# Kernel tuning notes

Measured on AMD Instinct MI355X. Metric: run time of the kernel, lower is better.

The kernel has to match this reference:

```python
import jax, jax.numpy as jnp
import numpy as np

HIDDEN = 128
N_NODES = 50000
N_EDGES = 640000


def setup_inputs() -> dict:
    key = jax.random.key(0)
    k1, k2, k3, k4, k5, k6, k7 = jax.random.split(key, 7)
    z = jax.random.normal(k1, (N_NODES, HIDDEN), dtype=jnp.float32)
    edge_index = jax.random.randint(k2, (2, N_EDGES), 0, N_NODES, dtype=jnp.int64)
    # Linear params (torch default uniform(-1/sqrt(fan_in), 1/sqrt(fan_in)))
    b1 = 1.0 / np.sqrt(2 * HIDDEN)
    W1 = jax.random.uniform(k3, (HIDDEN, 2 * HIDDEN), jnp.float32, -b1, b1)
    bias1 = jax.random.uniform(k4, (HIDDEN,), jnp.float32, -b1, b1)
    b2 = 1.0 / np.sqrt(HIDDEN)
    W2 = jax.random.uniform(k5, (1, HIDDEN), jnp.float32, -b2, b2)
    bias2 = jax.random.uniform(k6, (1,), jnp.float32, -b2, b2)
    return {"z": z, "W1": W1, "bias1": bias1, "W2": W2, "bias2": bias2,
            "edge_index": edge_index}


def reference(z, W1, bias1, W2, bias2, edge_index):
    # Gather endpoint embeddings: [E, H] each
    z_src = z[edge_index[0]]
    z_dst = z[edge_index[1]]
    h = jnp.concatenate([z_src, z_dst], axis=-1)  # [E, 2H]
    h = jax.nn.relu(h @ W1.T + bias1)             # [E, H]
    out = h @ W2.T + bias2                        # [E, 1]
    return out.reshape(-1)
```

## Files before the change

### kernel.cpp

```cpp
#include <hip/hip_runtime.h>
#include <hip/hip_bf16.h>


#define N_NODES 50000
#define N_EDGES 640000
#define H 128

using bf16 = __hip_bfloat16;
typedef __attribute__((ext_vector_type(8))) short short8;
typedef __attribute__((ext_vector_type(4))) float f32x4;

#define GLD_LDS16(g, l)                                                     \
  __builtin_amdgcn_global_load_lds(                                         \
      (const __attribute__((address_space(1))) void*)(g),                   \
      (__attribute__((address_space(3))) void*)(l), 16, 0, 0)

static __device__ __forceinline__ short bfbits(float x) {
  __hip_bfloat16 h = __float2bfloat16(x);
  return *reinterpret_cast<short*>(&h);
}

static __device__ __forceinline__ short8 pack8(float4 a, float4 b) {
  short8 r;
  r[0] = bfbits(a.x); r[1] = bfbits(a.y); r[2] = bfbits(a.z); r[3] = bfbits(a.w);
  r[4] = bfbits(b.x); r[5] = bfbits(b.y); r[6] = bfbits(b.z); r[7] = bfbits(b.w);
  return r;
}

__global__ __launch_bounds__(256) void w_to_bf16(const float* __restrict__ W1,
                                                 bf16* __restrict__ Wb) {
  const int u = blockIdx.x * 256 + threadIdx.x;
  const int o = u >> 4, k8 = (u & 15) * 8;
  const float4* src = reinterpret_cast<const float4*>(
      W1 + (size_t)(o & (H - 1)) * (2 * H) + (o >> 7) * H + k8);
  *reinterpret_cast<short8*>(Wb + (size_t)o * H + k8) = pack8(src[0], src[1]);
}

#define HP 136

__global__ __launch_bounds__(256) void precompute_uv(
    const float* __restrict__ z, const bf16* __restrict__ Wb,
    bf16* __restrict__ U, bf16* __restrict__ V) {
  __shared__ float ldsF[32 * H];
  __shared__ bf16 ldsH[32 * HP];
  const int tid = threadIdx.x;
  const int lane = tid & 63;
  const int s = tid >> 6;
  const int l15 = lane & 15, quad = lane >> 4;
  const int nodebase = blockIdx.x * 32;

  {
    int r0 = nodebase + s * 8;
    if (r0 > N_NODES - 8) r0 = N_NODES - 8;
    const float* gsrc = z + (size_t)r0 * H + lane * 4;
    float* ldst = ldsF + s * 8 * H;
#pragma unroll
    for (int j = 0; j < 4; ++j) GLD_LDS16(gsrc + j * 256, ldst + j * 256);
  }

  short8 wf[4][4];
#pragma unroll
  for (int t = 0; t < 4; ++t) {
    const bf16* wp = Wb + (size_t)(s * 64 + t * 16 + l15) * H + quad * 8;
#pragma unroll
    for (int q = 0; q < 4; ++q)
      wf[t][q] = *reinterpret_cast<const short8*>(wp + q * 32);
  }

  __syncthreads();

  {
    const int row = tid >> 3, off = (tid & 7) * 16;
    const float4* fp = reinterpret_cast<const float4*>(ldsF + row * H + off);
    const float4 a = fp[0], b = fp[1], c = fp[2], d = fp[3];
    *reinterpret_cast<short8*>(&ldsH[row * HP + off]) = pack8(a, b);
    *reinterpret_cast<short8*>(&ldsH[row * HP + off + 8]) = pack8(c, d);
  }
  __syncthreads();

  short8 zf[2][4];
#pragma unroll
  for (int m = 0; m < 2; ++m)
#pragma unroll
    for (int q = 0; q < 4; ++q)
      zf[m][q] = *reinterpret_cast<const short8*>(
          &ldsH[(m * 16 + l15) * HP + quad * 8 + q * 32]);

  f32x4 acc[2][4] = {};
#pragma unroll
  for (int m = 0; m < 2; ++m)
#pragma unroll
    for (int t = 0; t < 4; ++t)
#pragma unroll
      for (int q = 0; q < 4; ++q)
        acc[m][t] =
            __builtin_amdgcn_mfma_f32_16x16x32_bf16(wf[t][q], zf[m][q], acc[m][t], 0, 0, 0);

  bf16* epi = reinterpret_cast<bf16*>(ldsF);
#pragma unroll
  for (int m = 0; m < 2; ++m) {
    const int nl = m * 16 + l15;
#pragma unroll
    for (int t = 0; t < 4; ++t) {
      const int o = s * 64 + t * 16 + quad * 4;
      ushort4 st;
      st.x = (unsigned short)bfbits(acc[m][t][0]);
      st.y = (unsigned short)bfbits(acc[m][t][1]);
      st.z = (unsigned short)bfbits(acc[m][t][2]);
      st.w = (unsigned short)bfbits(acc[m][t][3]);
      *reinterpret_cast<ushort4*>(epi + nl * 256 + o) = st;
    }
  }
  __syncthreads();

#pragma unroll
  for (int half = 0; half < 2; ++half) {
    bf16* base = half ? V : U;
#pragma unroll
    for (int it = 0; it < 2; ++it) {
      const int nl = s * 8 + it * 4 + (lane >> 4);
      const int oc = (lane & 15) * 8;
      const short8 v = *reinterpret_cast<const short8*>(epi + nl * 256 + half * H + oc);
      const int n = nodebase + nl;
      if (n < N_NODES)
        *reinterpret_cast<short8*>(base + (size_t)n * H + oc) = v;
    }
  }
}

static __device__ __forceinline__ void acc2(unsigned u, unsigned v,
                                            float b1lo, float b1hi,
                                            float w2lo, float w2hi, float& sum) {
  const float ulo = __uint_as_float(u << 16);
  const float uhi = __uint_as_float(u & 0xffff0000u);
  const float vlo = __uint_as_float(v << 16);
  const float vhi = __uint_as_float(v & 0xffff0000u);
  float h0 = ulo + vlo + b1lo; h0 = fmaxf(h0, 0.f);
  float h1 = uhi + vhi + b1hi; h1 = fmaxf(h1, 0.f);
  sum = fmaf(h0, w2lo, sum);
  sum = fmaf(h1, w2hi, sum);
}

__global__ __launch_bounds__(256, 4) void edge_decode(
    const int* __restrict__ eidx, const bf16* __restrict__ Ub,
    const bf16* __restrict__ Vb, const float* __restrict__ bias1,
    const float* __restrict__ W2, const float* __restrict__ bias2,
    float* __restrict__ out) {
  const int lane = threadIdx.x & 63;
  const int w = blockIdx.x * 4 + (int)(threadIdx.x >> 6);
  const int chunk = w * 64;
  const int e8 = lane & 7;

  float b1r[16], w2r[16];
  const float4* bp = reinterpret_cast<const float4*>(bias1 + e8 * 16);
  const float4* wp = reinterpret_cast<const float4*>(W2 + e8 * 16);
#pragma unroll
  for (int q = 0; q < 4; ++q) {
    const float4 b = bp[q], wv = wp[q];
    b1r[q * 4 + 0] = b.x; b1r[q * 4 + 1] = b.y; b1r[q * 4 + 2] = b.z; b1r[q * 4 + 3] = b.w;
    w2r[q * 4 + 0] = wv.x; w2r[q * 4 + 1] = wv.y; w2r[q * 4 + 2] = wv.z; w2r[q * 4 + 3] = wv.w;
  }
  const float b2 = bias2[0];

  const int src = eidx[chunk + lane];
  const int dst = eidx[N_EDGES + chunk + lane];
  const uint4* U4 = reinterpret_cast<const uint4*>(Ub);
  const uint4* V4 = reinterpret_cast<const uint4*>(Vb);

  float res = 0.f;
#pragma unroll
  for (int half = 0; half < 2; ++half) {
    uint4 ua[4], ub[4], va[4], vb[4];
#pragma unroll
    for (int j = 0; j < 4; ++j) {
      const int i = half * 4 + j;
      const int sl = (lane & 56) + i;
      const int s_i = __shfl(src, sl);
      const int d_i = __shfl(dst, sl);
      const uint4* up = U4 + (size_t)s_i * 16 + e8 * 2;
      const uint4* vp = V4 + (size_t)d_i * 16 + e8 * 2;
      ua[j] = up[0]; ub[j] = up[1];
      va[j] = vp[0]; vb[j] = vp[1];
    }
#pragma unroll
    for (int j = 0; j < 4; ++j) {
      const int i = half * 4 + j;
      float sum = 0.f;
      acc2(ua[j].x, va[j].x, b1r[0],  b1r[1],  w2r[0],  w2r[1],  sum);
      acc2(ua[j].y, va[j].y, b1r[2],  b1r[3],  w2r[2],  w2r[3],  sum);
      acc2(ua[j].z, va[j].z, b1r[4],  b1r[5],  w2r[4],  w2r[5],  sum);
      acc2(ua[j].w, va[j].w, b1r[6],  b1r[7],  w2r[6],  w2r[7],  sum);
      acc2(ub[j].x, vb[j].x, b1r[8],  b1r[9],  w2r[8],  w2r[9],  sum);
      acc2(ub[j].y, vb[j].y, b1r[10], b1r[11], w2r[10], w2r[11], sum);
      acc2(ub[j].z, vb[j].z, b1r[12], b1r[13], w2r[12], w2r[13], sum);
      acc2(ub[j].w, vb[j].w, b1r[14], b1r[15], w2r[14], w2r[15], sum);
      sum += __shfl_xor(sum, 1);
      sum += __shfl_xor(sum, 2);
      sum += __shfl_xor(sum, 4);
      if (e8 == i) res = sum + b2;
    }
  }
  out[chunk + lane] = res;
}

extern "C" void kernel_launch(void* const* d_in, const int* in_sizes, int n_in,
                              void* d_out, int out_size, void* d_ws, size_t ws_size,
                              hipStream_t stream) {
  const float* z     = (const float*)d_in[0];
  const float* W1    = (const float*)d_in[1];
  const float* bias1 = (const float*)d_in[2];
  const float* W2    = (const float*)d_in[3];
  const float* bias2 = (const float*)d_in[4];
  const int*   eidx  = (const int*)d_in[5];
  float* out = (float*)d_out;

  bf16* U  = (bf16*)d_ws;
  bf16* V  = U + (size_t)N_NODES * H;
  bf16* Wb = V + (size_t)N_NODES * H;

  hipLaunchKernelGGL(w_to_bf16, dim3(16), dim3(256), 0, stream, W1, Wb);
  hipLaunchKernelGGL(precompute_uv, dim3((N_NODES + 31) / 32), dim3(256), 0, stream,
                     z, Wb, U, V);
  hipLaunchKernelGGL(edge_decode, dim3(N_EDGES / 64 / 4), dim3(256), 0, stream,
                     eidx, U, V, bias1, W2, bias2, out);
}
```

Measured before the change: 136.6 us.

## Bin edges by endpoint ranges and schedule decode per XCD for L2 locality

Adds a histogram, scan and scatter pass that buckets edges by coarse (dst, src) node ranges into 256 bins, packing src, dst and edge id into 64-bit records. The decode kernel then assigns each group of 32 bins to one XCD (blockIdx & 7) so each XCD's L2 sees a smaller working set of U/V rows, aiming to reduce random gather traffic to HBM. This costs three extra kernels, a memset and atomics, extra global traffic for the sorted records, and scattered output writes. It also assumes node ids fit in 16 bits and that blocks map round-robin to XCDs.

```diff
diff --git a/kernel.cpp b/kernel.cpp
--- a/kernel.cpp
+++ b/kernel.cpp
@@ -5,6 +5,11 @@
 #define N_NODES 50000
 #define N_EDGES 640000
 #define H 128
+
+#define NBINS 256
+#define S1_BLOCKS 128
+#define EPT 20
+#define P_XCD 64
 
 using bf16 = __hip_bfloat16;
 typedef __attribute__((ext_vector_type(8))) short short8;
@@ -124,6 +129,84 @@
       const int n = nodebase + nl;
       if (n < N_NODES)
         *reinterpret_cast<short8*>(base + (size_t)n * H + oc) = v;
+    }
+  }
+}
+
+
+static __device__ __forceinline__ int edge_key(int src, int dst) {
+  return (dst / 6250) * 32 + src / 1563;
+}
+
+__global__ __launch_bounds__(256) void edge_hist(const int* __restrict__ eidx,
+                                                 int* __restrict__ hist) {
+  __shared__ int lh[NBINS];
+  const int t = threadIdx.x;
+  lh[t] = 0;
+  __syncthreads();
+  const int base = blockIdx.x * (256 * EPT) + t;
+#pragma unroll
+  for (int j = 0; j < EPT; ++j) {
+    const int e = base + j * 256;
+    if (e < N_EDGES)
+      atomicAdd(&lh[edge_key(eidx[e], eidx[N_EDGES + e])], 1);
+  }
+  __syncthreads();
+  if (lh[t]) atomicAdd(&hist[t * 16], lh[t]);
+}
+
+__global__ __launch_bounds__(256) void edge_scan(const int* __restrict__ hist,
+                                                 int* __restrict__ cursors,
+                                                 int* __restrict__ xstart) {
+  __shared__ int sh[NBINS];
+  const int t = threadIdx.x;
+  const int v = hist[t * 16];
+  int acc = v;
+  sh[t] = acc;
+  for (int off = 1; off < NBINS; off <<= 1) {
+    __syncthreads();
+    const int add = (t >= off) ? sh[t - off] : 0;
+    __syncthreads();
+    acc += add;
+    sh[t] = acc;
+  }
+  const int excl = acc - v;
+  cursors[t * 16] = excl;
+  if ((t & 31) == 0) xstart[t >> 5] = excl;
+  if (t == 0) xstart[8] = N_EDGES;
+}
+
+__global__ __launch_bounds__(256) void edge_scatter(
+    const int* __restrict__ eidx, int* __restrict__ cursors,
+    unsigned long long* __restrict__ sde) {
+  __shared__ int lh[NBINS];
+  __shared__ int lcur[NBINS];
+  const int t = threadIdx.x;
+  lh[t] = 0;
+  __syncthreads();
+  int src[EPT], dst[EPT], key[EPT];
+  const int base = blockIdx.x * (256 * EPT) + t;
+#pragma unroll
+  for (int j = 0; j < EPT; ++j) {
+    const int e = base + j * 256;
+    if (e < N_EDGES) {
+      src[j] = eidx[e];
+      dst[j] = eidx[N_EDGES + e];
+      key[j] = edge_key(src[j], dst[j]);
+      atomicAdd(&lh[key[j]], 1);
+    } else {
+      key[j] = -1;
+    }
+  }
+  __syncthreads();
+  lcur[t] = lh[t] ? atomicAdd(&cursors[t * 16], lh[t]) : 0;
+  __syncthreads();
+#pragma unroll
+  for (int j = 0; j < EPT; ++j) {
+    if (key[j] >= 0) {
+      const int pos = atomicAdd(&lcur[key[j]], 1);
+      sde[pos] = ((unsigned long long)(unsigned)(base + j * 256) << 32) |
+                 ((unsigned)dst[j] << 16) | (unsigned)src[j];
     }
   }
 }
@@ -141,14 +224,12 @@
   sum = fmaf(h1, w2hi, sum);
 }
 
-__global__ __launch_bounds__(256, 4) void edge_decode(
-    const int* __restrict__ eidx, const bf16* __restrict__ Ub,
+__global__ __launch_bounds__(256, 4) void edge_decode_sorted(
+    const unsigned long long* __restrict__ sde, const bf16* __restrict__ Ub,
     const bf16* __restrict__ Vb, const float* __restrict__ bias1,
     const float* __restrict__ W2, const float* __restrict__ bias2,
-    float* __restrict__ out) {
+    const int* __restrict__ xstart, float* __restrict__ out) {
   const int lane = threadIdx.x & 63;
-  const int w = blockIdx.x * 4 + (int)(threadIdx.x >> 6);
-  const int chunk = w * 64;
   const int e8 = lane & 7;
 
   float b1r[16], w2r[16];
@@ -162,45 +243,56 @@
   }
   const float b2 = bias2[0];
 
-  const int src = eidx[chunk + lane];
-  const int dst = eidx[N_EDGES + chunk + lane];
+  const int xcd = blockIdx.x & 7;
+  const int slot = blockIdx.x >> 3;
+  const int xs = xstart[xcd], xe = xstart[xcd + 1];
   const uint4* U4 = reinterpret_cast<const uint4*>(Ub);
   const uint4* V4 = reinterpret_cast<const uint4*>(Vb);
 
-  float res = 0.f;
-#pragma unroll
-  for (int half = 0; half < 2; ++half) {
-    uint4 ua[4], ub[4], va[4], vb[4];
-#pragma unroll
-    for (int j = 0; j < 4; ++j) {
-      const int i = half * 4 + j;
-      const int sl = (lane & 56) + i;
-      const int s_i = __shfl(src, sl);
-      const int d_i = __shfl(dst, sl);
-      const uint4* up = U4 + (size_t)s_i * 16 + e8 * 2;
-      const uint4* vp = V4 + (size_t)d_i * 16 + e8 * 2;
-      ua[j] = up[0]; ub[j] = up[1];
-      va[j] = vp[0]; vb[j] = vp[1];
-    }
-#pragma unroll
-    for (int j = 0; j < 4; ++j) {
-      const int i = half * 4 + j;
-      float sum = 0.f;
-      acc2(ua[j].x, va[j].x, b1r[0],  b1r[1],  w2r[0],  w2r[1],  sum);
-      acc2(ua[j].y, va[j].y, b1r[2],  b1r[3],  w2r[2],  w2r[3],  sum);
-      acc2(ua[j].z, va[j].z, b1r[4],  b1r[5],  w2r[4],  w2r[5],  sum);
-      acc2(ua[j].w, va[j].w, b1r[6],  b1r[7],  w2r[6],  w2r[7],  sum);
-      acc2(ub[j].x, vb[j].x, b1r[8],  b1r[9],  w2r[8],  w2r[9],  sum);
-      acc2(ub[j].y, vb[j].y, b1r[10], b1r[11], w2r[10], w2r[11], sum);
-      acc2(ub[j].z, vb[j].z, b1r[12], b1r[13], w2r[12], w2r[13], sum);
-      acc2(ub[j].w, vb[j].w, b1r[14], b1r[15], w2r[14], w2r[15], sum);
-      sum += __shfl_xor(sum, 1);
-      sum += __shfl_xor(sum, 2);
-      sum += __shfl_xor(sum, 4);
-      if (e8 == i) res = sum + b2;
-    }
-  }
-  out[chunk + lane] = res;
+  for (int cb = xs + (slot * 4 + (int)(threadIdx.x >> 6)) * 64; cb < xe;
+       cb += P_XCD * 256) {
+    const int idx = cb + lane;
+    const bool valid = idx < xe;
+    const unsigned long long v = valid ? sde[idx] : 0ull;
+    const int src = (int)(v & 0xFFFFu);
+    const int dst = (int)((v >> 16) & 0xFFFFu);
+    const int eid = (int)(v >> 32);
+
+    float res = 0.f;
+#pragma unroll
+    for (int half = 0; half < 2; ++half) {
+      uint4 ua[4], ub[4], va[4], vb[4];
+#pragma unroll
+      for (int j = 0; j < 4; ++j) {
+        const int i = half * 4 + j;
+        const int sl = (lane & 56) + i;
+        const int s_i = __shfl(src, sl);
+        const int d_i = __shfl(dst, sl);
+        const uint4* up = U4 + (size_t)s_i * 16 + e8 * 2;
+        const uint4* vp = V4 + (size_t)d_i * 16 + e8 * 2;
+        ua[j] = up[0]; ub[j] = up[1];
+        va[j] = vp[0]; vb[j] = vp[1];
+      }
+#pragma unroll
+      for (int j = 0; j < 4; ++j) {
+        const int i = half * 4 + j;
+        float sum = 0.f;
+        acc2(ua[j].x, va[j].x, b1r[0],  b1r[1],  w2r[0],  w2r[1],  sum);
+        acc2(ua[j].y, va[j].y, b1r[2],  b1r[3],  w2r[2],  w2r[3],  sum);
+        acc2(ua[j].z, va[j].z, b1r[4],  b1r[5],  w2r[4],  w2r[5],  sum);
+        acc2(ua[j].w, va[j].w, b1r[6],  b1r[7],  w2r[6],  w2r[7],  sum);
+        acc2(ub[j].x, vb[j].x, b1r[8],  b1r[9],  w2r[8],  w2r[9],  sum);
+        acc2(ub[j].y, vb[j].y, b1r[10], b1r[11], w2r[10], w2r[11], sum);
+        acc2(ub[j].z, vb[j].z, b1r[12], b1r[13], w2r[12], w2r[13], sum);
+        acc2(ub[j].w, vb[j].w, b1r[14], b1r[15], w2r[14], w2r[15], sum);
+        sum += __shfl_xor(sum, 1);
+        sum += __shfl_xor(sum, 2);
+        sum += __shfl_xor(sum, 4);
+        if (e8 == i) res = sum + b2;
+      }
+    }
+    if (valid) out[eid] = res;
+  }
 }
 
 extern "C" void kernel_launch(void* const* d_in, const int* in_sizes, int n_in,
@@ -217,10 +309,20 @@
   bf16* U  = (bf16*)d_ws;
   bf16* V  = U + (size_t)N_NODES * H;
   bf16* Wb = V + (size_t)N_NODES * H;
+  unsigned long long* sde = (unsigned long long*)(Wb + 256 * H);
+  int* hist    = (int*)(sde + N_EDGES);
+  int* cursors = hist + NBINS * 16;
+  int* xstart  = cursors + NBINS * 16;
+
+  hipMemsetAsync(hist, 0, NBINS * 16 * sizeof(int), stream);
 
   hipLaunchKernelGGL(w_to_bf16, dim3(16), dim3(256), 0, stream, W1, Wb);
   hipLaunchKernelGGL(precompute_uv, dim3((N_NODES + 31) / 32), dim3(256), 0, stream,
                      z, Wb, U, V);
-  hipLaunchKernelGGL(edge_decode, dim3(N_EDGES / 64 / 4), dim3(256), 0, stream,
-                     eidx, U, V, bias1, W2, bias2, out);
-}
+  hipLaunchKernelGGL(edge_hist, dim3(S1_BLOCKS), dim3(256), 0, stream, eidx, hist);
+  hipLaunchKernelGGL(edge_scan, dim3(1), dim3(256), 0, stream, hist, cursors, xstart);
+  hipLaunchKernelGGL(edge_scatter, dim3(S1_BLOCKS), dim3(256), 0, stream,
+                     eidx, cursors, sde);
+  hipLaunchKernelGGL(edge_decode_sorted, dim3(8 * P_XCD), dim3(256), 0, stream,
+                     sde, U, V, bias1, W2, bias2, xstart, out);
+}
```

Result: slower. 154.8 us (+13.3%).

## Bucket edges by source node to reuse U rows in edge decoding

Applied to the files above, without the earlier changes.

Adds a bucketing kernel that groups edges by source node into fixed-capacity slots with an overflow list. The decode kernel then walks nodes in a grid-stride loop, loads each source U row once and reuses it across that node's edges, gathering only V rows per edge. The aim is to halve the random row gathers. In exchange it pays for a memset, atomics, an extra kernel and scattered output writes, and the per-node loop has divergent trip counts. Packing the destination index into 16 bits truncates node ids of 65536 and above; with 50000 nodes this holds.

```diff
diff --git a/kernel.cpp b/kernel.cpp
--- a/kernel.cpp
+++ b/kernel.cpp
@@ -5,6 +5,9 @@
 #define N_NODES 50000
 #define N_EDGES 640000
 #define H 128
+
+#define CAP 64
+#define OVF_MAX 65536
 
 using bf16 = __hip_bfloat16;
 typedef __attribute__((ext_vector_type(8))) short short8;
@@ -125,6 +128,25 @@
       if (n < N_NODES)
         *reinterpret_cast<short8*>(base + (size_t)n * H + oc) = v;
     }
+  }
+}
+
+__global__ __launch_bounds__(256) void build_buckets(
+    const int* __restrict__ eidx, int* __restrict__ cnt, int* __restrict__ ovfn,
+    unsigned long long* __restrict__ slots,
+    unsigned long long* __restrict__ ovfl) {
+  const int e = blockIdx.x * 256 + threadIdx.x;
+  if (e >= N_EDGES) return;
+  const unsigned s = (unsigned)eidx[e];
+  const unsigned d = (unsigned)eidx[N_EDGES + e];
+  const unsigned long long p =
+      ((unsigned long long)(unsigned)e << 32) | (d << 16) | s;
+  const int pos = atomicAdd(&cnt[s], 1);
+  if (pos < CAP) {
+    slots[(size_t)s * CAP + pos] = p;
+  } else {
+    const int op = atomicAdd(ovfn, 1);
+    if (op < OVF_MAX) ovfl[op] = p;
   }
 }
 
@@ -141,15 +163,30 @@
   sum = fmaf(h1, w2hi, sum);
 }
 
-__global__ __launch_bounds__(256, 4) void edge_decode(
-    const int* __restrict__ eidx, const bf16* __restrict__ Ub,
-    const bf16* __restrict__ Vb, const float* __restrict__ bias1,
-    const float* __restrict__ W2, const float* __restrict__ bias2,
-    float* __restrict__ out) {
-  const int lane = threadIdx.x & 63;
-  const int w = blockIdx.x * 4 + (int)(threadIdx.x >> 6);
-  const int chunk = w * 64;
-  const int e8 = lane & 7;
+static __device__ __forceinline__ float edge_sum(const uint4& a0, const uint4& a1,
+                                                 const uint4& c0, const uint4& c1,
+                                                 const float* b1r, const float* w2r) {
+  float sum = 0.f;
+  acc2(a0.x, c0.x, b1r[0],  b1r[1],  w2r[0],  w2r[1],  sum);
+  acc2(a0.y, c0.y, b1r[2],  b1r[3],  w2r[2],  w2r[3],  sum);
+  acc2(a0.z, c0.z, b1r[4],  b1r[5],  w2r[4],  w2r[5],  sum);
+  acc2(a0.w, c0.w, b1r[6],  b1r[7],  w2r[6],  w2r[7],  sum);
+  acc2(a1.x, c1.x, b1r[8],  b1r[9],  w2r[8],  w2r[9],  sum);
+  acc2(a1.y, c1.y, b1r[10], b1r[11], w2r[10], w2r[11], sum);
+  acc2(a1.z, c1.z, b1r[12], b1r[13], w2r[12], w2r[13], sum);
+  acc2(a1.w, c1.w, b1r[14], b1r[15], w2r[14], w2r[15], sum);
+  return sum;
+}
+
+__global__ __launch_bounds__(256, 4) void edge_decode_csr(
+    const unsigned long long* __restrict__ slots, const int* __restrict__ cnt,
+    const int* __restrict__ ovfn, const unsigned long long* __restrict__ ovfl,
+    const bf16* __restrict__ Ub, const bf16* __restrict__ Vb,
+    const float* __restrict__ bias1, const float* __restrict__ W2,
+    const float* __restrict__ bias2, float* __restrict__ out) {
+  const int e8 = threadIdx.x & 7;
+  const int g = (blockIdx.x * 256 + threadIdx.x) >> 3;
+  const int n_groups = gridDim.x * 32;
 
   float b1r[16], w2r[16];
   const float4* bp = reinterpret_cast<const float4*>(bias1 + e8 * 16);
@@ -162,45 +199,61 @@
   }
   const float b2 = bias2[0];
 
-  const int src = eidx[chunk + lane];
-  const int dst = eidx[N_EDGES + chunk + lane];
   const uint4* U4 = reinterpret_cast<const uint4*>(Ub);
   const uint4* V4 = reinterpret_cast<const uint4*>(Vb);
 
-  float res = 0.f;
-#pragma unroll
-  for (int half = 0; half < 2; ++half) {
-    uint4 ua[4], ub[4], va[4], vb[4];
-#pragma unroll
-    for (int j = 0; j < 4; ++j) {
-      const int i = half * 4 + j;
-      const int sl = (lane & 56) + i;
-      const int s_i = __shfl(src, sl);
-      const int d_i = __shfl(dst, sl);
-      const uint4* up = U4 + (size_t)s_i * 16 + e8 * 2;
-      const uint4* vp = V4 + (size_t)d_i * 16 + e8 * 2;
-      ua[j] = up[0]; ub[j] = up[1];
-      va[j] = vp[0]; vb[j] = vp[1];
+  for (int n = g; n < N_NODES; n += n_groups) {
+    const int deg = min(cnt[n], CAP);
+    if (deg == 0) continue;
+    const uint4* up = U4 + (size_t)n * 16 + e8 * 2;
+    const uint4 u0 = up[0], u1 = up[1];
+    const unsigned long long* sb = slots + (size_t)n * CAP;
+
+    for (int j0 = 0; j0 < deg; j0 += 4) {
+      const int m = deg - j0;
+      unsigned long long ent = 0;
+      if ((e8 & 3) < m) ent = sb[j0 + (e8 & 3)];
+      uint4 va[4], vb[4];
+      int eid[4];
+#pragma unroll
+      for (int j = 0; j < 4; ++j) {
+        const unsigned long long pj = __shfl(ent, (threadIdx.x & 56) | j);
+        if (j < m) {
+          const int dj = (int)((pj >> 16) & 0xffffu);
+          eid[j] = (int)(pj >> 32);
+          const uint4* vp = V4 + (size_t)dj * 16 + e8 * 2;
+          va[j] = vp[0];
+          vb[j] = vp[1];
+        }
+      }
+#pragma unroll
+      for (int j = 0; j < 4; ++j) {
+        if (j < m) {
+          float sum = edge_sum(u0, u1, va[j], vb[j], b1r, w2r);
+          sum += __shfl_xor(sum, 1);
+          sum += __shfl_xor(sum, 2);
+          sum += __shfl_xor(sum, 4);
+          if (e8 == j) out[eid[j]] = sum + b2;
+        }
+      }
     }
-#pragma unroll
-    for (int j = 0; j < 4; ++j) {
-      const int i = half * 4 + j;
-      float sum = 0.f;
-      acc2(ua[j].x, va[j].x, b1r[0],  b1r[1],  w2r[0],  w2r[1],  sum);
-      acc2(ua[j].y, va[j].y, b1r[2],  b1r[3],  w2r[2],  w2r[3],  sum);
-      acc2(ua[j].z, va[j].z, b1r[4],  b1r[5],  w2r[4],  w2r[5],  sum);
-      acc2(ua[j].w, va[j].w, b1r[6],  b1r[7],  w2r[6],  w2r[7],  sum);
-      acc2(ub[j].x, vb[j].x, b1r[8],  b1r[9],  w2r[8],  w2r[9],  sum);
-      acc2(ub[j].y, vb[j].y, b1r[10], b1r[11], w2r[10], w2r[11], sum);
-      acc2(ub[j].z, vb[j].z, b1r[12], b1r[13], w2r[12], w2r[13], sum);
-      acc2(ub[j].w, vb[j].w, b1r[14], b1r[15], w2r[14], w2r[15], sum);
-      sum += __shfl_xor(sum, 1);
-      sum += __shfl_xor(sum, 2);
-      sum += __shfl_xor(sum, 4);
-      if (e8 == i) res = sum + b2;
-    }
-  }
-  out[chunk + lane] = res;
+  }
+
+  const int no = min(*ovfn, OVF_MAX);
+  for (int i = g; i < no; i += n_groups) {
+    const unsigned long long p = ovfl[i];
+    const int s = (int)(p & 0xffffu);
+    const int d = (int)((p >> 16) & 0xffffu);
+    const int eid0 = (int)(p >> 32);
+    const uint4* up2 = U4 + (size_t)s * 16 + e8 * 2;
+    const uint4* vp2 = V4 + (size_t)d * 16 + e8 * 2;
+    const uint4 a0 = up2[0], a1 = up2[1], c0 = vp2[0], c1 = vp2[1];
+    float sum = edge_sum(a0, a1, c0, c1, b1r, w2r);
+    sum += __shfl_xor(sum, 1);
+    sum += __shfl_xor(sum, 2);
+    sum += __shfl_xor(sum, 4);
+    if (e8 == 0) out[eid0] = sum + b2;
+  }
 }
 
 extern "C" void kernel_launch(void* const* d_in, const int* in_sizes, int n_in,
@@ -217,10 +270,20 @@
   bf16* U  = (bf16*)d_ws;
   bf16* V  = U + (size_t)N_NODES * H;
   bf16* Wb = V + (size_t)N_NODES * H;
+  unsigned long long* slots =
+      (unsigned long long*)(Wb + 256 * H);
+  int* cnt  = (int*)(slots + (size_t)N_NODES * CAP);
+  int* ovfn = cnt + 50048;
+  unsigned long long* ovfl =
+      (unsigned long long*)(cnt + 50064);
+
+  hipMemsetAsync(cnt, 0, 50064 * sizeof(int), stream);
 
   hipLaunchKernelGGL(w_to_bf16, dim3(16), dim3(256), 0, stream, W1, Wb);
   hipLaunchKernelGGL(precompute_uv, dim3((N_NODES + 31) / 32), dim3(256), 0, stream,
                      z, Wb, U, V);
-  hipLaunchKernelGGL(edge_decode, dim3(N_EDGES / 64 / 4), dim3(256), 0, stream,
-                     eidx, U, V, bias1, W2, bias2, out);
-}
+  hipLaunchKernelGGL(build_buckets, dim3((N_EDGES + 255) / 256), dim3(256), 0,
+                     stream, eidx, cnt, ovfn, slots, ovfl);
+  hipLaunchKernelGGL(edge_decode_csr, dim3(512), dim3(256), 0, stream,
+                     slots, cnt, ovfn, ovfl, U, V, bias1, W2, bias2, out);
+}
```

Result: slower. 202.7 us (+48.3%).

## Bin edges by src/dst node range and map bins to XCDs for L2 locality

Applied to the files above, without the earlier changes.

Adds a scatter pass that buckets edges into 256 bins keyed by destination and source node ranges, packing src, dst and edge id into 64-bit entries. The W conversion is folded into the same launch. The decode kernel then processes bins with block-to-XCD mapping so each XCD's L2 sees a limited slice of the U/V tables, and an overflow list catches bins that exceed capacity. The aim is to raise cache hit rates on the random U/V gathers, at the cost of an extra pass over edges, atomics, a memset and scattered output writes.

```diff
diff --git a/kernel.cpp b/kernel.cpp
--- a/kernel.cpp
+++ b/kernel.cpp
@@ -5,6 +5,13 @@
 #define N_NODES 50000
 #define N_EDGES 640000
 #define H 128
+
+#define NBINS 256
+#define CAPB 3072
+#define CHUNKS_PER_BIN 12
+#define SCAT_BLOCKS 128
+#define EPT 20
+#define OVF_MAX 65536
 
 using bf16 = __hip_bfloat16;
 typedef __attribute__((ext_vector_type(8))) short short8;
@@ -25,15 +32,6 @@
   r[0] = bfbits(a.x); r[1] = bfbits(a.y); r[2] = bfbits(a.z); r[3] = bfbits(a.w);
   r[4] = bfbits(b.x); r[5] = bfbits(b.y); r[6] = bfbits(b.z); r[7] = bfbits(b.w);
   return r;
-}
-
-__global__ __launch_bounds__(256) void w_to_bf16(const float* __restrict__ W1,
-                                                 bf16* __restrict__ Wb) {
-  const int u = blockIdx.x * 256 + threadIdx.x;
-  const int o = u >> 4, k8 = (u & 15) * 8;
-  const float4* src = reinterpret_cast<const float4*>(
-      W1 + (size_t)(o & (H - 1)) * (2 * H) + (o >> 7) * H + k8);
-  *reinterpret_cast<short8*>(Wb + (size_t)o * H + k8) = pack8(src[0], src[1]);
 }
 
 #define HP 136
@@ -124,6 +122,57 @@
       const int n = nodebase + nl;
       if (n < N_NODES)
         *reinterpret_cast<short8*>(base + (size_t)n * H + oc) = v;
+    }
+  }
+}
+
+__global__ __launch_bounds__(256) void scatter_w(
+    const int* __restrict__ eidx, const float* __restrict__ W1,
+    bf16* __restrict__ Wb, int* __restrict__ cursors, int* __restrict__ ovfn,
+    unsigned long long* __restrict__ sde,
+    unsigned long long* __restrict__ ovfl) {
+  if (blockIdx.x >= SCAT_BLOCKS) {
+    const int u = (blockIdx.x - SCAT_BLOCKS) * 256 + threadIdx.x;
+    const int o = u >> 4, k8 = (u & 15) * 8;
+    const float4* src = reinterpret_cast<const float4*>(
+        W1 + (size_t)(o & (H - 1)) * (2 * H) + (o >> 7) * H + k8);
+    *reinterpret_cast<short8*>(Wb + (size_t)o * H + k8) = pack8(src[0], src[1]);
+    return;
+  }
+  __shared__ int lh[NBINS];
+  __shared__ int lcur[NBINS];
+  const int t = threadIdx.x;
+  lh[t] = 0;
+  __syncthreads();
+  unsigned long long ent[EPT];
+  int key[EPT];
+  const int base = blockIdx.x * (256 * EPT) + t;
+#pragma unroll
+  for (int j = 0; j < EPT; ++j) {
+    const int e = base + j * 256;
+    if (e < N_EDGES) {
+      const unsigned s = (unsigned)eidx[e];
+      const unsigned d = (unsigned)eidx[N_EDGES + e];
+      ent[j] = ((unsigned long long)(unsigned)e << 32) | (d << 16) | s;
+      key[j] = (int)(d / 6250u) * 32 + (int)(s / 1563u);
+      atomicAdd(&lh[key[j]], 1);
+    } else {
+      key[j] = -1;
+    }
+  }
+  __syncthreads();
+  lcur[t] = lh[t] ? atomicAdd(&cursors[t * 16], lh[t]) : 0;
+  __syncthreads();
+#pragma unroll
+  for (int j = 0; j < EPT; ++j) {
+    if (key[j] >= 0) {
+      const int pos = atomicAdd(&lcur[key[j]], 1);
+      if (pos < CAPB) {
+        sde[(size_t)key[j] * CAPB + pos] = ent[j];
+      } else {
+        const int op = atomicAdd(ovfn, 1);
+        if (op < OVF_MAX) ovfl[op] = ent[j];
+      }
     }
   }
 }
@@ -141,31 +190,31 @@
   sum = fmaf(h1, w2hi, sum);
 }
 
-__global__ __launch_bounds__(256, 4) void edge_decode(
-    const int* __restrict__ eidx, const bf16* __restrict__ Ub,
-    const bf16* __restrict__ Vb, const float* __restrict__ bias1,
-    const float* __restrict__ W2, const float* __restrict__ bias2,
-    float* __restrict__ out) {
-  const int lane = threadIdx.x & 63;
-  const int w = blockIdx.x * 4 + (int)(threadIdx.x >> 6);
-  const int chunk = w * 64;
-  const int e8 = lane & 7;
-
-  float b1r[16], w2r[16];
-  const float4* bp = reinterpret_cast<const float4*>(bias1 + e8 * 16);
-  const float4* wp = reinterpret_cast<const float4*>(W2 + e8 * 16);
-#pragma unroll
-  for (int q = 0; q < 4; ++q) {
-    const float4 b = bp[q], wv = wp[q];
-    b1r[q * 4 + 0] = b.x; b1r[q * 4 + 1] = b.y; b1r[q * 4 + 2] = b.z; b1r[q * 4 + 3] = b.w;
-    w2r[q * 4 + 0] = wv.x; w2r[q * 4 + 1] = wv.y; w2r[q * 4 + 2] = wv.z; w2r[q * 4 + 3] = wv.w;
-  }
-  const float b2 = bias2[0];
-
-  const int src = eidx[chunk + lane];
-  const int dst = eidx[N_EDGES + chunk + lane];
-  const uint4* U4 = reinterpret_cast<const uint4*>(Ub);
-  const uint4* V4 = reinterpret_cast<const uint4*>(Vb);
+static __device__ __forceinline__ float edge_sum(const uint4& a0, const uint4& a1,
+                                                 const uint4& c0, const uint4& c1,
+                                                 const float* b1r, const float* w2r) {
+  float sum = 0.f;
+  acc2(a0.x, c0.x, b1r[0],  b1r[1],  w2r[0],  w2r[1],  sum);
+  acc2(a0.y, c0.y, b1r[2],  b1r[3],  w2r[2],  w2r[3],  sum);
+  acc2(a0.z, c0.z, b1r[4],  b1r[5],  w2r[4],  w2r[5],  sum);
+  acc2(a0.w, c0.w, b1r[6],  b1r[7],  w2r[6],  w2r[7],  sum);
+  acc2(a1.x, c1.x, b1r[8],  b1r[9],  w2r[8],  w2r[9],  sum);
+  acc2(a1.y, c1.y, b1r[10], b1r[11], w2r[10], w2r[11], sum);
+  acc2(a1.z, c1.z, b1r[12], b1r[13], w2r[12], w2r[13], sum);
+  acc2(a1.w, c1.w, b1r[14], b1r[15], w2r[14], w2r[15], sum);
+  return sum;
+}
+
+static __device__ __forceinline__ void decode64(
+    const unsigned long long* __restrict__ ents, int mvalid,
+    const uint4* __restrict__ U4, const uint4* __restrict__ V4,
+    const float* b1r, const float* w2r, float b2, float* __restrict__ out,
+    int lane, int e8) {
+  const bool valid = lane < mvalid;
+  const unsigned long long v = valid ? ents[lane] : 0ull;
+  const int src = (int)(v & 0xffffu);
+  const int dst = (int)((v >> 16) & 0xffffu);
+  const int eid = (int)(v >> 32);
 
   float res = 0.f;
 #pragma unroll
@@ -174,7 +223,7 @@
 #pragma unroll
     for (int j = 0; j < 4; ++j) {
       const int i = half * 4 + j;
-      const int sl = (lane & 56) + i;
+      const int sl = (lane & 56) | i;
       const int s_i = __shfl(src, sl);
       const int d_i = __shfl(dst, sl);
       const uint4* up = U4 + (size_t)s_i * 16 + e8 * 2;
@@ -185,22 +234,54 @@
 #pragma unroll
     for (int j = 0; j < 4; ++j) {
       const int i = half * 4 + j;
-      float sum = 0.f;
-      acc2(ua[j].x, va[j].x, b1r[0],  b1r[1],  w2r[0],  w2r[1],  sum);
-      acc2(ua[j].y, va[j].y, b1r[2],  b1r[3],  w2r[2],  w2r[3],  sum);
-      acc2(ua[j].z, va[j].z, b1r[4],  b1r[5],  w2r[4],  w2r[5],  sum);
-      acc2(ua[j].w, va[j].w, b1r[6],  b1r[7],  w2r[6],  w2r[7],  sum);
-      acc2(ub[j].x, vb[j].x, b1r[8],  b1r[9],  w2r[8],  w2r[9],  sum);
-      acc2(ub[j].y, vb[j].y, b1r[10], b1r[11], w2r[10], w2r[11], sum);
-      acc2(ub[j].z, vb[j].z, b1r[12], b1r[13], w2r[12], w2r[13], sum);
-      acc2(ub[j].w, vb[j].w, b1r[14], b1r[15], w2r[14], w2r[15], sum);
+      float sum = edge_sum(ua[j], ub[j], va[j], vb[j], b1r, w2r);
       sum += __shfl_xor(sum, 1);
       sum += __shfl_xor(sum, 2);
       sum += __shfl_xor(sum, 4);
       if (e8 == i) res = sum + b2;
     }
   }
-  out[chunk + lane] = res;
+  if (valid) out[eid] = res;
+}
+
+__global__ __launch_bounds__(256, 4) void edge_decode_sorted(
+    const unsigned long long* __restrict__ sde, const int* __restrict__ cursors,
+    const int* __restrict__ ovfn, const unsigned long long* __restrict__ ovfl,
+    const bf16* __restrict__ Ub, const bf16* __restrict__ Vb,
+    const float* __restrict__ bias1, const float* __restrict__ W2,
+    const float* __restrict__ bias2, float* __restrict__ out) {
+  const int lane = threadIdx.x & 63;
+  const int e8 = lane & 7;
+  const int w = threadIdx.x >> 6;
+
+  float b1r[16], w2r[16];
+  const float4* bp = reinterpret_cast<const float4*>(bias1 + e8 * 16);
+  const float4* wp = reinterpret_cast<const float4*>(W2 + e8 * 16);
+#pragma unroll
+  for (int q = 0; q < 4; ++q) {
+    const float4 b = bp[q], wv = wp[q];
+    b1r[q * 4 + 0] = b.x; b1r[q * 4 + 1] = b.y; b1r[q * 4 + 2] = b.z; b1r[q * 4 + 3] = b.w;
+    w2r[q * 4 + 0] = wv.x; w2r[q * 4 + 1] = wv.y; w2r[q * 4 + 2] = wv.z; w2r[q * 4 + 3] = wv.w;
+  }
+  const float b2 = bias2[0];
+
+  const uint4* U4 = reinterpret_cast<const uint4*>(Ub);
+  const uint4* V4 = reinterpret_cast<const uint4*>(Vb);
+
+  const int xcd = blockIdx.x & 7;
+  const int slot = blockIdx.x >> 3;
+  const int sb = slot / CHUNKS_PER_BIN;
+  const int k = slot - sb * CHUNKS_PER_BIN;
+  const int bin = (xcd << 5) + sb;
+  const int c = min(cursors[bin * 16], CAPB);
+  const int base = k * 256 + w * 64;
+  if (base < c)
+    decode64(sde + (size_t)bin * CAPB + base, min(64, c - base), U4, V4, b1r,
+             w2r, b2, out, lane, e8);
+
+  const int no = min(*ovfn, OVF_MAX);
+  for (int b0 = (blockIdx.x * 4 + w) * 64; b0 < no; b0 += (int)gridDim.x * 4 * 64)
+    decode64(ovfl + b0, min(64, no - b0), U4, V4, b1r, w2r, b2, out, lane, e8);
 }
 
 extern "C" void kernel_launch(void* const* d_in, const int* in_sizes, int n_in,
@@ -217,10 +298,20 @@
   bf16* U  = (bf16*)d_ws;
   bf16* V  = U + (size_t)N_NODES * H;
   bf16* Wb = V + (size_t)N_NODES * H;
-
-  hipLaunchKernelGGL(w_to_bf16, dim3(16), dim3(256), 0, stream, W1, Wb);
+  unsigned long long* sde =
+      (unsigned long long*)(Wb + 256 * H);
+  int* cursors = (int*)(sde + (size_t)NBINS * CAPB);
+  int* ovfn    = cursors + NBINS * 16;
+  unsigned long long* ovfl =
+      (unsigned long long*)(cursors + NBINS * 16 + 16);
+
+  hipMemsetAsync(cursors, 0, (NBINS * 16 + 16) * sizeof(int), stream);
+
+  hipLaunchKernelGGL(scatter_w, dim3(SCAT_BLOCKS + 16), dim3(256), 0, stream,
+                     eidx, W1, Wb, cursors, ovfn, sde, ovfl);
   hipLaunchKernelGGL(precompute_uv, dim3((N_NODES + 31) / 32), dim3(256), 0, stream,
                      z, Wb, U, V);
-  hipLaunchKernelGGL(edge_decode, dim3(N_EDGES / 64 / 4), dim3(256), 0, stream,
-                     eidx, U, V, bias1, W2, bias2, out);
-}
+  hipLaunchKernelGGL(edge_decode_sorted, dim3(8 * 32 * CHUNKS_PER_BIN), dim3(256),
+                     0, stream, sde, cursors, ovfn, ovfl, U, V, bias1, W2, bias2,
+                     out);
+}
```

New measurement: 144.6 us. +5.8%, slower.
